# Optimization experiments

Measured on AMD Instinct MI355X. Metric: run time of the kernel, lower is better.

## Reference

```python
import jax, jax.numpy as jnp
import numpy as np

EMBED_DIM = 768
NUM_HEADS = 12
HEAD_DIM = EMBED_DIM // NUM_HEADS
B, S = 2, 2048


def setup_inputs() -> dict:
    key = jax.random.key(0)
    k1, k2, k3, k4, k5 = jax.random.split(key, 5)
    scale = 1.0 / np.sqrt(EMBED_DIM)
    return {
        "x": jax.random.normal(k1, (B, S, EMBED_DIM), dtype=jnp.float32),
        "w_qkv": jax.random.normal(k2, (EMBED_DIM, 3 * EMBED_DIM), dtype=jnp.float32) * scale,
        "b_qkv": jax.random.normal(k3, (3 * EMBED_DIM,), dtype=jnp.float32) * 0.01,
        "w_proj": jax.random.normal(k4, (EMBED_DIM, EMBED_DIM), dtype=jnp.float32) * scale,
        "b_proj": jax.random.normal(k5, (EMBED_DIM,), dtype=jnp.float32) * 0.01,
    }


def reference(x, w_qkv, b_qkv, w_proj, b_proj):
    b, s, e = x.shape
    h, d = NUM_HEADS, HEAD_DIM
    # fused QKV projection: [b, s, 3, h, d]
    qkv = (x @ w_qkv + b_qkv).reshape(b, s, 3, h, d)
    q = qkv[:, :, 0].transpose(0, 2, 1, 3)  # [b, h, s, d]
    k = qkv[:, :, 1].transpose(0, 2, 1, 3)
    v = qkv[:, :, 2].transpose(0, 2, 1, 3)
    scores = jnp.einsum("bhqd,bhkd->bhqk", q, k) * (d ** -0.5)
    attn = jax.nn.softmax(scores, axis=-1)  # dropout is identity in eval mode
    out = jnp.einsum("bhqk,bhkd->bhqd", attn, v)
    out = out.transpose(0, 2, 1, 3).reshape(b, s, e)
    return out @ w_proj + b_proj
```

## Files before the change

kernel.cpp:

```cpp
#include <hip/hip_runtime.h>
#include <hip/hip_bf16.h>


typedef __bf16 bf16x8 __attribute__((ext_vector_type(8)));
typedef float f32x4 __attribute__((ext_vector_type(4)));
typedef unsigned short ushortx8 __attribute__((ext_vector_type(8)));
typedef unsigned short ushortx4 __attribute__((ext_vector_type(4)));

#define EMB 768
#define SEQ 2048
#define NBATCH 2
#define NHEAD 12
#define HDIM 64
#define MROWS (NBATCH*SEQ)
#define NQKV (3*EMB)

static __device__ __forceinline__ unsigned short b16(float f) {
  __hip_bfloat16 h = __float2bfloat16(f);
  return __builtin_bit_cast(unsigned short, h);
}

static __device__ __forceinline__ void gld16(const void* g, void* l) {
  __builtin_amdgcn_global_load_lds((const __attribute__((address_space(1))) void*)g,
                                   (__attribute__((address_space(3))) void*)l, 16, 0, 0);
}

__global__ __launch_bounds__(256) void k_cvt_bf16(const float* __restrict__ in,
                                                  unsigned short* __restrict__ out, int n) {
  int i = (blockIdx.x * 256 + threadIdx.x) * 4;
  if (i >= n) return;
  f32x4 v = *(const f32x4*)(in + i);
  ushortx4 o;
  o[0] = b16(v[0]); o[1] = b16(v[1]); o[2] = b16(v[2]); o[3] = b16(v[3]);
  *(ushortx4*)(out + i) = o;
}

__global__ __launch_bounds__(256) void k_tcvt(const float* __restrict__ in,
                                              unsigned short* __restrict__ out,
                                              int K, int N) {
  __shared__ float t[64][65];
  const int n0 = blockIdx.x * 64, k0 = blockIdx.y * 64;
  const int x = threadIdx.x & 63, y0 = threadIdx.x >> 6;
  #pragma unroll
  for (int i = 0; i < 16; ++i) {
    int r = y0 * 16 + i;
    t[r][x] = in[(size_t)(k0 + r) * N + n0 + x];
  }
  __syncthreads();
  #pragma unroll
  for (int i = 0; i < 16; ++i) {
    int r = y0 * 16 + i;
    out[(size_t)(n0 + r) * K + k0 + x] = b16(t[x][r]);
  }
}

static __device__ __forceinline__ void gemm_tile_128(
    const unsigned short* __restrict__ A, const unsigned short* __restrict__ B,
    int K, int bm, int bn, unsigned short* Alds, unsigned short* Blds, f32x4 acc[4][4]) {
  const int tid = threadIdx.x;
  const int lane = tid & 63, w = tid >> 6;
  const int l15 = lane & 15, lg = lane >> 4;
  const int wm = w >> 1, wn = w & 1;
  #pragma unroll
  for (int m = 0; m < 4; ++m)
    #pragma unroll
    for (int n = 0; n < 4; ++n)
      acc[m][n] = (f32x4){0.f, 0.f, 0.f, 0.f};

  const size_t aoff1 = (size_t)(bm * 128 + (tid >> 2)) * K + (tid & 3) * 8;
  const size_t aoff2 = (size_t)(bm * 128 + (tid >> 2) + 64) * K + (tid & 3) * 8;
  const size_t boff1 = (size_t)(bn * 128 + (tid >> 2)) * K + (tid & 3) * 8;
  const size_t boff2 = (size_t)(bn * 128 + (tid >> 2) + 64) * K + (tid & 3) * 8;
  char* lA = (char*)Alds;
  char* lB = (char*)Blds;
  const char* aBase = (const char*)Alds + (wm * 64 + l15) * 64 + lg * 16;
  const char* bBase = (const char*)Blds + (wn * 64 + l15) * 64 + lg * 16;

  gld16(A + aoff1, lA + w * 1024);
  gld16(A + aoff2, lA + 4096 + w * 1024);
  gld16(B + boff1, lB + w * 1024);
  gld16(B + boff2, lB + 4096 + w * 1024);

  const int T = K >> 5;
  for (int t = 0; t < T; ++t) {
    const int cur = t & 1;
    if (t + 1 < T) {
      const int k1 = (t + 1) << 5;
      char* ad = lA + (cur ^ 1) * 8192 + w * 1024;
      char* bd = lB + (cur ^ 1) * 8192 + w * 1024;
      gld16(A + aoff1 + k1, ad);
      gld16(A + aoff2 + k1, ad + 4096);
      gld16(B + boff1 + k1, bd);
      gld16(B + boff2 + k1, bd + 4096);
      asm volatile("s_waitcnt vmcnt(4)" ::: "memory");
    } else {
      asm volatile("s_waitcnt vmcnt(0)" ::: "memory");
    }
    __builtin_amdgcn_s_barrier();
    const char* ab = aBase + cur * 8192;
    const char* bb = bBase + cur * 8192;
    bf16x8 af[4], bfr[4];
    #pragma unroll
    for (int m = 0; m < 4; ++m) af[m] = *(const bf16x8*)(ab + m * 1024);
    #pragma unroll
    for (int n = 0; n < 4; ++n) bfr[n] = *(const bf16x8*)(bb + n * 1024);
    #pragma unroll
    for (int m = 0; m < 4; ++m)
      #pragma unroll
      for (int n = 0; n < 4; ++n)
        acc[m][n] = __builtin_amdgcn_mfma_f32_16x16x32_bf16(af[m], bfr[n], acc[m][n], 0, 0, 0);
    if (t + 1 < T) __builtin_amdgcn_s_barrier();
  }
}

#define QSCALE 0.18033688011112042f
__global__ __launch_bounds__(256) void k_gemm_qkv(
    const unsigned short* __restrict__ Xb, const unsigned short* __restrict__ Wt,
    const float* __restrict__ bias,
    unsigned short* __restrict__ Qb, unsigned short* __restrict__ Kb,
    unsigned short* __restrict__ VTb) {
  __shared__ __align__(16) unsigned short Alds[2 * 128 * 32];
  __shared__ __align__(16) unsigned short Blds[2 * 128 * 32];
  f32x4 acc[4][4];
  const int bm = blockIdx.x, bn = blockIdx.y;
  gemm_tile_128(Xb, Wt, EMB, bm, bn, Alds, Blds, acc);
  const int tid = threadIdx.x, lane = tid & 63, w = tid >> 6;
  const int l15 = lane & 15, lg = lane >> 4, wm = w >> 1, wn = w & 1;
  #pragma unroll
  for (int m = 0; m < 4; ++m)
    #pragma unroll
    for (int n = 0; n < 4; ++n)
      #pragma unroll
      for (int r = 0; r < 4; ++r) {
        int gr = bm * 128 + wm * 64 + m * 16 + lg * 4 + r;
        int gc = bn * 128 + wn * 64 + n * 16 + l15;
        float v = acc[m][n][r] + bias[gc];
        int t = gc / 768, rem = gc % 768;
        int h = rem >> 6, d = rem & 63;
        int b = gr >> 11, s = gr & 2047;
        int bh = b * 12 + h;
        if (t == 0)      Qb[((size_t)bh * 2048 + s) * 64 + d] = b16(v * QSCALE);
        else if (t == 1) Kb[((size_t)bh * 2048 + s) * 64 + d] = b16(v);
        else {
          int sp = (s & ~0x1C) | ((s & 0x0C) << 1) | ((s & 0x10) >> 2);
          VTb[((size_t)bh * 64 + d) * 2048 + sp] = b16(v);
        }
      }
}

__global__ __launch_bounds__(256) void k_gemm_proj(
    const unsigned short* __restrict__ Ab, const unsigned short* __restrict__ Wt,
    const float* __restrict__ bias, float* __restrict__ out) {
  __shared__ __align__(16) unsigned short Alds[2 * 128 * 32];
  __shared__ __align__(16) unsigned short Blds[2 * 128 * 32];
  f32x4 acc[4][4];
  const int bm = blockIdx.x, bn = blockIdx.y;
  gemm_tile_128(Ab, Wt, EMB, bm, bn, Alds, Blds, acc);
  const int tid = threadIdx.x, lane = tid & 63, w = tid >> 6;
  const int l15 = lane & 15, lg = lane >> 4, wm = w >> 1, wn = w & 1;
  #pragma unroll
  for (int m = 0; m < 4; ++m)
    #pragma unroll
    for (int n = 0; n < 4; ++n)
      #pragma unroll
      for (int r = 0; r < 4; ++r) {
        int gr = bm * 128 + wm * 64 + m * 16 + lg * 4 + r;
        int gc = bn * 128 + wn * 64 + n * 16 + l15;
        out[(size_t)gr * EMB + gc] = acc[m][n][r] + bias[gc];
      }
}

__global__ __launch_bounds__(256) void k_attn(
    const unsigned short* __restrict__ Qg, const unsigned short* __restrict__ Kg,
    const unsigned short* __restrict__ VTg, unsigned short* __restrict__ AO) {
  __shared__ __align__(16) char KL[2 * 8192];
  __shared__ __align__(16) char VTL[2 * 8192];
  const int bid = blockIdx.x;
  const int bh = bid >> 5, qt = bid & 31;
  const int b = bh / 12, h = bh % 12;
  const size_t base = (size_t)bh * (SEQ * HDIM);
  const int tid = threadIdx.x, lane = tid & 63, w = tid >> 6;
  const int l15 = lane & 15, lg = lane >> 4;
  const int swz = (l15 & 7) << 4;

  bf16x8 qf[2];
  {
    const size_t qoff = base + (size_t)(qt * 64 + w * 16 + l15) * 64 + lg * 8;
    qf[0] = *(const bf16x8*)(Qg + qoff);
    qf[1] = *(const bf16x8*)(Qg + qoff + 32);
  }

  const int srow0 = tid >> 3;
  const int scg0 = (tid & 7) ^ (srow0 & 7);
  const int scg1 = (tid & 7) ^ ((srow0 + 32) & 7);

  f32x4 Oacc[4];
  #pragma unroll
  for (int nd = 0; nd < 4; ++nd) Oacc[nd] = (f32x4){0.f, 0.f, 0.f, 0.f};
  float l_ = 0.f;

  gld16(Kg + base + (size_t)srow0 * 64 + scg0 * 8,            KL + w * 1024);
  gld16(Kg + base + (size_t)(srow0 + 32) * 64 + scg1 * 8,     KL + 4096 + w * 1024);
  gld16(VTg + base + (size_t)srow0 * 2048 + scg0 * 8,         VTL + w * 1024);
  gld16(VTg + base + (size_t)(srow0 + 32) * 2048 + scg1 * 8,  VTL + 4096 + w * 1024);
  __syncthreads();

  for (int t = 0; t < 32; ++t) {
    const int bi = t & 1;
    if (t < 31) {
      const int kv1 = (t + 1) * 64;
      char* kd = KL + (bi ^ 1) * 8192 + w * 1024;
      char* vd = VTL + (bi ^ 1) * 8192 + w * 1024;
      gld16(Kg + base + (size_t)(kv1 + srow0) * 64 + scg0 * 8,           kd);
      gld16(Kg + base + (size_t)(kv1 + srow0 + 32) * 64 + scg1 * 8,      kd + 4096);
      gld16(VTg + base + (size_t)srow0 * 2048 + kv1 + scg0 * 8,          vd);
      gld16(VTg + base + (size_t)(srow0 + 32) * 2048 + kv1 + scg1 * 8,   vd + 4096);
    }
    const char* kb = KL + bi * 8192;
    const char* vb = VTL + bi * 8192;

    f32x4 sv[4];
    __builtin_amdgcn_s_setprio(1);
    #pragma unroll
    for (int n = 0; n < 4; ++n) {
      const char* rb = kb + (n * 16 + l15) * 128;
      bf16x8 kf0 = *(const bf16x8*)(rb + ((lg * 16) ^ swz));
      bf16x8 kf1 = *(const bf16x8*)(rb + ((64 + lg * 16) ^ swz));
      f32x4 z = (f32x4){0.f, 0.f, 0.f, 0.f};
      z = __builtin_amdgcn_mfma_f32_16x16x32_bf16(kf0, qf[0], z, 0, 0, 0);
      sv[n] = __builtin_amdgcn_mfma_f32_16x16x32_bf16(kf1, qf[1], z, 0, 0, 0);
    }

    #pragma unroll
    for (int c = 0; c < 2; ++c) {
      ushortx8 up;
      #pragma unroll
      for (int j = 0; j < 4; ++j) {
        float pa = __builtin_amdgcn_exp2f(sv[2 * c][j]);
        float pb = __builtin_amdgcn_exp2f(sv[2 * c + 1][j]);
        l_ += pa + pb;
        up[j] = b16(pa);
        up[4 + j] = b16(pb);
      }
      bf16x8 pfB = __builtin_bit_cast(bf16x8, up);
      #pragma unroll
      for (int nd = 0; nd < 4; ++nd) {
        const char* vr = vb + (nd * 16 + l15) * 128;
        bf16x8 vf = *(const bf16x8*)(vr + ((c * 64 + lg * 16) ^ swz));
        Oacc[nd] = __builtin_amdgcn_mfma_f32_16x16x32_bf16(vf, pfB, Oacc[nd], 0, 0, 0);
      }
    }
    __builtin_amdgcn_s_setprio(0);
    __syncthreads();
  }

  l_ += __shfl_xor(l_, 16);
  l_ += __shfl_xor(l_, 32);
  const float rl = 1.0f / l_;
  const int q = qt * 64 + w * 16 + l15;
  #pragma unroll
  for (int nd = 0; nd < 4; ++nd) {
    ushortx4 o;
    #pragma unroll
    for (int r = 0; r < 4; ++r) o[r] = b16(Oacc[nd][r] * rl);
    *(ushortx4*)(AO + ((size_t)(b * 2048 + q)) * EMB + h * 64 + nd * 16 + lg * 4) = o;
  }
}

extern "C" void kernel_launch(void* const* d_in, const int* in_sizes, int n_in,
                              void* d_out, int out_size, void* d_ws, size_t ws_size,
                              hipStream_t stream) {
  const float* x     = (const float*)d_in[0];
  const float* wqkv  = (const float*)d_in[1];
  const float* bqkv  = (const float*)d_in[2];
  const float* wproj = (const float*)d_in[3];
  const float* bproj = (const float*)d_in[4];
  float* out = (float*)d_out;
  char* ws = (char*)d_ws;

  unsigned short* xb     = (unsigned short*)(ws + 0);
  unsigned short* wqkvT  = (unsigned short*)(ws + 6291456);
  unsigned short* wprojT = (unsigned short*)(ws + 9830400);
  unsigned short* Qb     = (unsigned short*)(ws + 11010048);
  unsigned short* Kb     = (unsigned short*)(ws + 17301504);
  unsigned short* VTb    = (unsigned short*)(ws + 23592960);
  unsigned short* AOb    = (unsigned short*)(ws + 29884416);

  k_cvt_bf16<<<3072, 256, 0, stream>>>(x, xb, MROWS * EMB);
  k_tcvt<<<dim3(NQKV / 64, EMB / 64), 256, 0, stream>>>(wqkv, wqkvT, EMB, NQKV);
  k_tcvt<<<dim3(EMB / 64, EMB / 64), 256, 0, stream>>>(wproj, wprojT, EMB, EMB);
  k_gemm_qkv<<<dim3(MROWS / 128, NQKV / 128), 256, 0, stream>>>(xb, wqkvT, bqkv, Qb, Kb, VTb);
  k_attn<<<24 * (SEQ / 64), 256, 0, stream>>>(Qb, Kb, VTb, AOb);
  k_gemm_proj<<<dim3(MROWS / 128, EMB / 128), 256, 0, stream>>>(AOb, wprojT, bproj, out);
}
```

Measured before the change: 99.24 us.

## Triple-buffer GEMM and attention loads, fuse prep kernels, vectorize V^T stores

Moves the GEMM tile loop and the attention KV loop from double to triple LDS buffering. Each iteration now prefetches two stages ahead and needs only one barrier instead of two. The three conversion and transpose kernels are merged into one launch, and the V^T epilogue writes four bf16 values per store instead of scalar stores. The extra LDS per block may lower occupancy.

```diff
diff --git a/kernel.cpp b/kernel.cpp
--- a/kernel.cpp
+++ b/kernel.cpp
@@ -9,11 +9,11 @@
 
 #define EMB 768
 #define SEQ 2048
-#define NBATCH 2
 #define NHEAD 12
 #define HDIM 64
-#define MROWS (NBATCH*SEQ)
-#define NQKV (3*EMB)
+#define MROWS 4096
+#define NQKV 2304
+#define QSCALE 0.18033688011112042f
 
 static __device__ __forceinline__ unsigned short b16(float f) {
   __hip_bfloat16 h = __float2bfloat16(f);
@@ -25,40 +25,36 @@
                                    (__attribute__((address_space(3))) void*)l, 16, 0, 0);
 }
 
-__global__ __launch_bounds__(256) void k_cvt_bf16(const float* __restrict__ in,
-                                                  unsigned short* __restrict__ out, int n) {
-  int i = (blockIdx.x * 256 + threadIdx.x) * 4;
-  if (i >= n) return;
-  f32x4 v = *(const f32x4*)(in + i);
-  ushortx4 o;
-  o[0] = b16(v[0]); o[1] = b16(v[1]); o[2] = b16(v[2]); o[3] = b16(v[3]);
-  *(ushortx4*)(out + i) = o;
-}
-
-__global__ __launch_bounds__(256) void k_tcvt(const float* __restrict__ in,
-                                              unsigned short* __restrict__ out,
-                                              int K, int N) {
+__global__ __launch_bounds__(256) void k_prep(
+    const float* __restrict__ x, const float* __restrict__ wqkv, const float* __restrict__ wproj,
+    unsigned short* __restrict__ xb, unsigned short* __restrict__ wqkvT,
+    unsigned short* __restrict__ wprojT) {
   __shared__ float t[64][65];
-  const int n0 = blockIdx.x * 64, k0 = blockIdx.y * 64;
-  const int x = threadIdx.x & 63, y0 = threadIdx.x >> 6;
-  #pragma unroll
-  for (int i = 0; i < 16; ++i) {
-    int r = y0 * 16 + i;
-    t[r][x] = in[(size_t)(k0 + r) * N + n0 + x];
-  }
+  const int bid = blockIdx.x;
+  if (bid < 3072) {
+    int i = (bid * 256 + threadIdx.x) * 4;
+    f32x4 v = *(const f32x4*)(x + i);
+    ushortx4 o;
+    o[0] = b16(v[0]); o[1] = b16(v[1]); o[2] = b16(v[2]); o[3] = b16(v[3]);
+    *(ushortx4*)(xb + i) = o;
+    return;
+  }
+  const float* in; unsigned short* out; int N, bx, by;
+  if (bid < 3072 + 432) { in = wqkv;  out = wqkvT;  N = NQKV; int r = bid - 3072; bx = r % 36; by = r / 36; }
+  else                  { in = wproj; out = wprojT; N = EMB;  int r = bid - 3504; bx = r % 12; by = r / 12; }
+  const int n0 = bx * 64, k0 = by * 64;
+  const int xx = threadIdx.x & 63, y0 = threadIdx.x >> 6;
+  #pragma unroll
+  for (int i = 0; i < 16; ++i) { int r = y0 * 16 + i; t[r][xx] = in[(size_t)(k0 + r) * N + n0 + xx]; }
   __syncthreads();
   #pragma unroll
-  for (int i = 0; i < 16; ++i) {
-    int r = y0 * 16 + i;
-    out[(size_t)(n0 + r) * K + k0 + x] = b16(t[x][r]);
-  }
+  for (int i = 0; i < 16; ++i) { int r = y0 * 16 + i; out[(size_t)(n0 + r) * EMB + k0 + xx] = b16(t[xx][r]); }
 }
 
 static __device__ __forceinline__ void gemm_tile_128(
     const unsigned short* __restrict__ A, const unsigned short* __restrict__ B,
-    int K, int bm, int bn, unsigned short* Alds, unsigned short* Blds, f32x4 acc[4][4]) {
-  const int tid = threadIdx.x;
-  const int lane = tid & 63, w = tid >> 6;
+    int K, int bm, int bn, char* lA, char* lB, f32x4 acc[4][4]) {
+  const int tid = threadIdx.x, lane = tid & 63, w = tid >> 6;
   const int l15 = lane & 15, lg = lane >> 4;
   const int wm = w >> 1, wn = w & 1;
   #pragma unroll
@@ -68,35 +64,31 @@
       acc[m][n] = (f32x4){0.f, 0.f, 0.f, 0.f};
 
   const size_t aoff1 = (size_t)(bm * 128 + (tid >> 2)) * K + (tid & 3) * 8;
-  const size_t aoff2 = (size_t)(bm * 128 + (tid >> 2) + 64) * K + (tid & 3) * 8;
+  const size_t aoff2 = aoff1 + (size_t)64 * K;
   const size_t boff1 = (size_t)(bn * 128 + (tid >> 2)) * K + (tid & 3) * 8;
-  const size_t boff2 = (size_t)(bn * 128 + (tid >> 2) + 64) * K + (tid & 3) * 8;
-  char* lA = (char*)Alds;
-  char* lB = (char*)Blds;
-  const char* aBase = (const char*)Alds + (wm * 64 + l15) * 64 + lg * 16;
-  const char* bBase = (const char*)Blds + (wn * 64 + l15) * 64 + lg * 16;
-
-  gld16(A + aoff1, lA + w * 1024);
-  gld16(A + aoff2, lA + 4096 + w * 1024);
-  gld16(B + boff1, lB + w * 1024);
-  gld16(B + boff2, lB + 4096 + w * 1024);
-
+  const size_t boff2 = boff1 + (size_t)64 * K;
+  const char* aBase = lA + (wm * 64 + l15) * 64 + lg * 16;
+  const char* bBase = lB + (wn * 64 + l15) * 64 + lg * 16;
   const int T = K >> 5;
+
+  #define GSTAGE(tt, buf) do {                                   \
+    char* ad_ = lA + (buf) * 8192 + w * 1024;                    \
+    char* bd_ = lB + (buf) * 8192 + w * 1024;                    \
+    const int k0_ = (tt) << 5;                                   \
+    gld16(A + aoff1 + k0_, ad_);                                 \
+    gld16(A + aoff2 + k0_, ad_ + 4096);                          \
+    gld16(B + boff1 + k0_, bd_);                                 \
+    gld16(B + boff2 + k0_, bd_ + 4096);                          \
+  } while (0)
+
+  GSTAGE(0, 0);
+  GSTAGE(1, 1);
+  asm volatile("s_waitcnt vmcnt(4)" ::: "memory");
+  __builtin_amdgcn_s_barrier();
+
+  int cur = 0, pre = 2;
   for (int t = 0; t < T; ++t) {
-    const int cur = t & 1;
-    if (t + 1 < T) {
-      const int k1 = (t + 1) << 5;
-      char* ad = lA + (cur ^ 1) * 8192 + w * 1024;
-      char* bd = lB + (cur ^ 1) * 8192 + w * 1024;
-      gld16(A + aoff1 + k1, ad);
-      gld16(A + aoff2 + k1, ad + 4096);
-      gld16(B + boff1 + k1, bd);
-      gld16(B + boff2 + k1, bd + 4096);
-      asm volatile("s_waitcnt vmcnt(4)" ::: "memory");
-    } else {
-      asm volatile("s_waitcnt vmcnt(0)" ::: "memory");
-    }
-    __builtin_amdgcn_s_barrier();
+    if (t + 2 < T) GSTAGE(t + 2, pre);
     const char* ab = aBase + cur * 8192;
     const char* bb = bBase + cur * 8192;
     bf16x8 af[4], bfr[4];
@@ -104,55 +96,82 @@
     for (int m = 0; m < 4; ++m) af[m] = *(const bf16x8*)(ab + m * 1024);
     #pragma unroll
     for (int n = 0; n < 4; ++n) bfr[n] = *(const bf16x8*)(bb + n * 1024);
+    __builtin_amdgcn_s_setprio(1);
     #pragma unroll
     for (int m = 0; m < 4; ++m)
       #pragma unroll
       for (int n = 0; n < 4; ++n)
         acc[m][n] = __builtin_amdgcn_mfma_f32_16x16x32_bf16(af[m], bfr[n], acc[m][n], 0, 0, 0);
-    if (t + 1 < T) __builtin_amdgcn_s_barrier();
-  }
-}
-
-#define QSCALE 0.18033688011112042f
+    __builtin_amdgcn_s_setprio(0);
+    if (t + 1 < T) {
+      if (t + 2 < T) asm volatile("s_waitcnt vmcnt(4)" ::: "memory");
+      else           asm volatile("s_waitcnt vmcnt(0)" ::: "memory");
+      __builtin_amdgcn_s_barrier();
+    }
+    cur = (cur == 2) ? 0 : cur + 1;
+    pre = (pre == 2) ? 0 : pre + 1;
+  }
+  #undef GSTAGE
+}
+
+static __device__ __forceinline__ int kvperm(int s) {
+  return (s & ~0x1C) | ((s & 0x0C) << 1) | ((s & 0x10) >> 2);
+}
+
 __global__ __launch_bounds__(256) void k_gemm_qkv(
     const unsigned short* __restrict__ Xb, const unsigned short* __restrict__ Wt,
     const float* __restrict__ bias,
     unsigned short* __restrict__ Qb, unsigned short* __restrict__ Kb,
     unsigned short* __restrict__ VTb) {
-  __shared__ __align__(16) unsigned short Alds[2 * 128 * 32];
-  __shared__ __align__(16) unsigned short Blds[2 * 128 * 32];
+  __shared__ __align__(16) char Alds[3 * 8192];
+  __shared__ __align__(16) char Blds[3 * 8192];
   f32x4 acc[4][4];
   const int bm = blockIdx.x, bn = blockIdx.y;
   gemm_tile_128(Xb, Wt, EMB, bm, bn, Alds, Blds, acc);
   const int tid = threadIdx.x, lane = tid & 63, w = tid >> 6;
   const int l15 = lane & 15, lg = lane >> 4, wm = w >> 1, wn = w & 1;
-  #pragma unroll
-  for (int m = 0; m < 4; ++m)
-    #pragma unroll
-    for (int n = 0; n < 4; ++n)
-      #pragma unroll
-      for (int r = 0; r < 4; ++r) {
-        int gr = bm * 128 + wm * 64 + m * 16 + lg * 4 + r;
+  const int treg = bn / 6;
+  if (treg < 2) {
+    #pragma unroll
+    for (int m = 0; m < 4; ++m)
+      #pragma unroll
+      for (int n = 0; n < 4; ++n)
+        #pragma unroll
+        for (int r = 0; r < 4; ++r) {
+          int gr = bm * 128 + wm * 64 + m * 16 + lg * 4 + r;
+          int gc = bn * 128 + wn * 64 + n * 16 + l15;
+          float v = acc[m][n][r] + bias[gc];
+          int rem = gc - treg * 768;
+          int h = rem >> 6, d = rem & 63;
+          int b = gr >> 11, s = gr & 2047;
+          size_t off = ((size_t)(b * 12 + h) * 2048 + s) * 64 + d;
+          if (treg == 0) Qb[off] = b16(v * QSCALE);
+          else           Kb[off] = b16(v);
+        }
+  } else {
+    #pragma unroll
+    for (int m = 0; m < 4; ++m)
+      #pragma unroll
+      for (int n = 0; n < 4; ++n) {
+        int gr0 = bm * 128 + wm * 64 + m * 16 + lg * 4;
         int gc = bn * 128 + wn * 64 + n * 16 + l15;
-        float v = acc[m][n][r] + bias[gc];
-        int t = gc / 768, rem = gc % 768;
+        int rem = gc - 1536;
         int h = rem >> 6, d = rem & 63;
-        int b = gr >> 11, s = gr & 2047;
-        int bh = b * 12 + h;
-        if (t == 0)      Qb[((size_t)bh * 2048 + s) * 64 + d] = b16(v * QSCALE);
-        else if (t == 1) Kb[((size_t)bh * 2048 + s) * 64 + d] = b16(v);
-        else {
-          int sp = (s & ~0x1C) | ((s & 0x0C) << 1) | ((s & 0x10) >> 2);
-          VTb[((size_t)bh * 64 + d) * 2048 + sp] = b16(v);
-        }
+        int b = gr0 >> 11, s0 = gr0 & 2047;
+        int sp0 = kvperm(s0);
+        ushortx4 o;
+        #pragma unroll
+        for (int r = 0; r < 4; ++r) o[r] = b16(acc[m][n][r] + bias[gc]);
+        *(ushortx4*)(VTb + ((size_t)(b * 12 + h) * 64 + d) * 2048 + sp0) = o;
       }
+  }
 }
 
 __global__ __launch_bounds__(256) void k_gemm_proj(
     const unsigned short* __restrict__ Ab, const unsigned short* __restrict__ Wt,
     const float* __restrict__ bias, float* __restrict__ out) {
-  __shared__ __align__(16) unsigned short Alds[2 * 128 * 32];
-  __shared__ __align__(16) unsigned short Blds[2 * 128 * 32];
+  __shared__ __align__(16) char Alds[3 * 8192];
+  __shared__ __align__(16) char Blds[3 * 8192];
   f32x4 acc[4][4];
   const int bm = blockIdx.x, bn = blockIdx.y;
   gemm_tile_128(Ab, Wt, EMB, bm, bn, Alds, Blds, acc);
@@ -173,8 +192,8 @@
 __global__ __launch_bounds__(256) void k_attn(
     const unsigned short* __restrict__ Qg, const unsigned short* __restrict__ Kg,
     const unsigned short* __restrict__ VTg, unsigned short* __restrict__ AO) {
-  __shared__ __align__(16) char KL[2 * 8192];
-  __shared__ __align__(16) char VTL[2 * 8192];
+  __shared__ __align__(16) char KL[3 * 8192];
+  __shared__ __align__(16) char VTL[3 * 8192];
   const int bid = blockIdx.x;
   const int bh = bid >> 5, qt = bid & 31;
   const int b = bh / 12, h = bh % 12;
@@ -194,30 +213,31 @@
   const int scg0 = (tid & 7) ^ (srow0 & 7);
   const int scg1 = (tid & 7) ^ ((srow0 + 32) & 7);
 
+  #define ASTAGE(tt, buf) do {                                                         \
+    const int kv_ = (tt) * 64;                                                         \
+    char* kd_ = KL + (buf) * 8192 + w * 1024;                                          \
+    char* vd_ = VTL + (buf) * 8192 + w * 1024;                                         \
+    gld16(Kg + base + (size_t)(kv_ + srow0) * 64 + scg0 * 8,           kd_);           \
+    gld16(Kg + base + (size_t)(kv_ + srow0 + 32) * 64 + scg1 * 8,      kd_ + 4096);    \
+    gld16(VTg + base + (size_t)srow0 * 2048 + kv_ + scg0 * 8,          vd_);           \
+    gld16(VTg + base + (size_t)(srow0 + 32) * 2048 + kv_ + scg1 * 8,   vd_ + 4096);    \
+  } while (0)
+
   f32x4 Oacc[4];
   #pragma unroll
   for (int nd = 0; nd < 4; ++nd) Oacc[nd] = (f32x4){0.f, 0.f, 0.f, 0.f};
   float l_ = 0.f;
 
-  gld16(Kg + base + (size_t)srow0 * 64 + scg0 * 8,            KL + w * 1024);
-  gld16(Kg + base + (size_t)(srow0 + 32) * 64 + scg1 * 8,     KL + 4096 + w * 1024);
-  gld16(VTg + base + (size_t)srow0 * 2048 + scg0 * 8,         VTL + w * 1024);
-  gld16(VTg + base + (size_t)(srow0 + 32) * 2048 + scg1 * 8,  VTL + 4096 + w * 1024);
-  __syncthreads();
-
+  ASTAGE(0, 0);
+  ASTAGE(1, 1);
+  asm volatile("s_waitcnt vmcnt(4)" ::: "memory");
+  __builtin_amdgcn_s_barrier();
+
+  int cur = 0, pre = 2;
   for (int t = 0; t < 32; ++t) {
-    const int bi = t & 1;
-    if (t < 31) {
-      const int kv1 = (t + 1) * 64;
-      char* kd = KL + (bi ^ 1) * 8192 + w * 1024;
-      char* vd = VTL + (bi ^ 1) * 8192 + w * 1024;
-      gld16(Kg + base + (size_t)(kv1 + srow0) * 64 + scg0 * 8,           kd);
-      gld16(Kg + base + (size_t)(kv1 + srow0 + 32) * 64 + scg1 * 8,      kd + 4096);
-      gld16(VTg + base + (size_t)srow0 * 2048 + kv1 + scg0 * 8,          vd);
-      gld16(VTg + base + (size_t)(srow0 + 32) * 2048 + kv1 + scg1 * 8,   vd + 4096);
-    }
-    const char* kb = KL + bi * 8192;
-    const char* vb = VTL + bi * 8192;
+    if (t + 2 < 32) ASTAGE(t + 2, pre);
+    const char* kb = KL + cur * 8192;
+    const char* vb = VTL + cur * 8192;
 
     f32x4 sv[4];
     __builtin_amdgcn_s_setprio(1);
@@ -251,8 +271,16 @@
       }
     }
     __builtin_amdgcn_s_setprio(0);
-    __syncthreads();
-  }
+
+    if (t < 31) {
+      if (t < 30) asm volatile("s_waitcnt vmcnt(4)" ::: "memory");
+      else        asm volatile("s_waitcnt vmcnt(0)" ::: "memory");
+      __builtin_amdgcn_s_barrier();
+    }
+    cur = (cur == 2) ? 0 : cur + 1;
+    pre = (pre == 2) ? 0 : pre + 1;
+  }
+  #undef ASTAGE
 
   l_ += __shfl_xor(l_, 16);
   l_ += __shfl_xor(l_, 32);
@@ -286,9 +314,7 @@
   unsigned short* VTb    = (unsigned short*)(ws + 23592960);
   unsigned short* AOb    = (unsigned short*)(ws + 29884416);
 
-  k_cvt_bf16<<<3072, 256, 0, stream>>>(x, xb, MROWS * EMB);
-  k_tcvt<<<dim3(NQKV / 64, EMB / 64), 256, 0, stream>>>(wqkv, wqkvT, EMB, NQKV);
-  k_tcvt<<<dim3(EMB / 64, EMB / 64), 256, 0, stream>>>(wproj, wprojT, EMB, EMB);
+  k_prep<<<3648, 256, 0, stream>>>(x, wqkv, wproj, xb, wqkvT, wprojT);
   k_gemm_qkv<<<dim3(MROWS / 128, NQKV / 128), 256, 0, stream>>>(xb, wqkvT, bqkv, Qb, Kb, VTb);
   k_attn<<<24 * (SEQ / 64), 256, 0, stream>>>(Qb, Kb, VTb, AOb);
   k_gemm_proj<<<dim3(MROWS / 128, EMB / 128), 256, 0, stream>>>(AOb, wprojT, bproj, out);
```

Measured after the change: 106.6 us. 1.07x slower.
